# Performance work log

Hardware: AMD Instinct MI355X
Metric: run time of the kernel (lower is better)

## Reference

```python
import jax, jax.numpy as jnp
import numpy as np

EPS = 2e-5
N_ROT = 4  # p4 group: rotations by multiples of 90 degrees (exact via rot90)


def _conv2d(x, w, pad):
    # x: [B, Cin, H, W], w: [Cout, Cin, k, k]
    return jax.lax.conv_general_dilated(
        x, w, window_strides=(1, 1), padding=[(pad, pad), (pad, pad)],
        dimension_numbers=('NCHW', 'OIHW', 'NCHW'))


def _conv_rng(x, w):
    # Lifting (Rn -> G) conv. x: [B, I, H, W], w: [O, I, k, k] -> [B, O, 4, H', W']
    O, I, k, _ = w.shape
    wr = jnp.stack([jnp.rot90(w, r, axes=(-2, -1)) for r in range(N_ROT)])  # [4,O,I,k,k]
    y = _conv2d(x, wr.reshape(N_ROT * O, I, k, k), 0)  # [B, 4*O, H', W']
    B, _, H2, W2 = y.shape
    return y.reshape(B, N_ROT, O, H2, W2).transpose(0, 2, 1, 3, 4)


def _conv_gg(x, w, pad=0):
    # Group (G -> G) conv. x: [B, I, 4, H, W], w: [O, I, 4, k, k] -> [B, O, 4, H', W']
    O, I, _, k, _ = w.shape
    ws = []
    for r in range(N_ROT):
        wr = jnp.rot90(w, r, axes=(-2, -1))      # spatial rotation of the kernel
        wr = jnp.roll(wr, r, axis=2)              # cyclic shift of orientation axis
        ws.append(wr.reshape(O, I * N_ROT, k, k))
    wall = jnp.concatenate(ws, 0)                 # [4*O, I*4, k, k]
    B = x.shape[0]
    y = _conv2d(x.reshape(B, I * N_ROT, x.shape[-2], x.shape[-1]), wall, pad)
    H2, W2 = y.shape[-2:]
    return y.reshape(B, N_ROT, O, H2, W2).transpose(0, 2, 1, 3, 4)


def _att_rng(x, aw):
    # fSpatialAttention on Rn input: channel avg+max pooling -> 7x7 conv -> sigmoid gate.
    # x: [B, C, H, W], aw: [1, 2, 7, 7]
    pooled = jnp.concatenate([x.mean(1, keepdims=True), x.max(1, keepdims=True)], axis=1)
    att = jax.nn.sigmoid(_conv2d(pooled, aw, 3))  # [B,1,H,W], SAME padding
    return x * att


def _att_gg(x, aw):
    # fSpatialAttentionGG on G input: channel avg+max pooling -> equivariant 7x7 GG conv -> sigmoid.
    # x: [B, C, 4, H, W], aw: [1, 2, 4, 7, 7]
    pooled = jnp.concatenate([x.mean(1, keepdims=True), x.max(1, keepdims=True)], axis=1)
    att = jax.nn.sigmoid(_conv_gg(pooled, aw, pad=3))  # [B,1,4,H,W]
    return x * att


def _bn(x, g, b):
    # BatchNorm3d over [B, C, 4, H, W]: per-channel stats over (B, 4, H, W)
    m = x.mean((0, 2, 3, 4), keepdims=True)
    v = x.var((0, 2, 3, 4), keepdims=True)
    return (x - m) * jax.lax.rsqrt(v + EPS) * g.reshape(1, -1, 1, 1, 1) + b.reshape(1, -1, 1, 1, 1)


def _pool(x):
    # max_pooling_Rn: 2x2/2 spatial max pool applied independently per orientation
    return jax.lax.reduce_window(x, -jnp.inf, jax.lax.max,
                                 (1, 1, 1, 2, 2), (1, 1, 1, 2, 2), 'VALID')


def setup_inputs() -> dict:
    key = jax.random.key(0)
    ks = jax.random.split(key, 40)
    B, C = 2048, 10
    d = {'x': jax.random.normal(ks[0], (B, 1, 28, 28), jnp.float32)}
    d['c1_w'] = 0.2 * jax.random.normal(ks[1], (C, 1, 3, 3), jnp.float32)
    d['a1_w'] = 0.1 * jax.random.normal(ks[2], (1, 2, 7, 7), jnp.float32)
    j = 3
    for i in range(2, 7):
        d['c%d_w' % i] = 0.1 * jax.random.normal(ks[j], (C, C, 4, 3, 3), jnp.float32); j += 1
        d['a%d_w' % i] = 0.1 * jax.random.normal(ks[j], (1, 2, 4, 7, 7), jnp.float32); j += 1
    d['c7_w'] = 0.1 * jax.random.normal(ks[j], (10, C, 4, 4, 4), jnp.float32); j += 1
    d['a7_w'] = 0.1 * jax.random.normal(ks[j], (1, 2, 4, 7, 7), jnp.float32); j += 1
    for i in range(1, 7):
        d['bn%d_g' % i] = jnp.ones((C,), jnp.float32)
        d['bn%d_b' % i] = jnp.zeros((C,), jnp.float32)
    return d


def reference(x, c1_w, a1_w, c2_w, a2_w, c3_w, a3_w, c4_w, a4_w, c5_w, a5_w,
              c6_w, a6_w, c7_w, a7_w, bn1_g, bn1_b, bn2_g, bn2_b, bn3_g, bn3_b,
              bn4_g, bn4_b, bn5_g, bn5_b, bn6_g, bn6_b):
    # Dropout is treated as identity (eval mode / deterministic reference).
    out = jax.nn.relu(_bn(_conv_rng(_att_rng(x, a1_w), c1_w), bn1_g, bn1_b))      # [B,10,4,26,26]
    out = jax.nn.relu(_bn(_conv_gg(_att_gg(out, a2_w), c2_w), bn2_g, bn2_b))       # [B,10,4,24,24]
    out = _pool(out)                                                                # [B,10,4,12,12]
    out = jax.nn.relu(_bn(_conv_gg(_att_gg(out, a3_w), c3_w), bn3_g, bn3_b))       # 10x10
    out = jax.nn.relu(_bn(_conv_gg(_att_gg(out, a4_w), c4_w), bn4_g, bn4_b))       # 8x8
    out = jax.nn.relu(_bn(_conv_gg(_att_gg(out, a5_w), c5_w), bn5_g, bn5_b))       # 6x6
    out = jax.nn.relu(_bn(_conv_gg(_att_gg(out, a6_w), c6_w), bn6_g, bn6_b))       # 4x4
    out = _conv_gg(_att_gg(out, a7_w), c7_w)                                        # [B,10,4,1,1]
    out = out.max(axis=2)                                                           # group max-pool over orientations
    return out.reshape(out.shape[0], 10)
```

## Files before the change

kernel.cpp:

```cpp
#include <hip/hip_runtime.h>
#include <hip/hip_bf16.h>
#include <cstddef>

typedef __hip_bfloat16 bf;
typedef __attribute__((ext_vector_type(8))) short short8x;
typedef __attribute__((ext_vector_type(4))) float f32x4;

__device__ __forceinline__ float ldv(const float* p){ return *p; }
__device__ __forceinline__ float ldv(const bf* p){ return __bfloat162float(*p); }
__device__ __forceinline__ void stv(float* p, float v){ *p = v; }
__device__ __forceinline__ void stv(bf* p, float v){ *p = __float2bfloat16(v); }
__device__ __forceinline__ float sigm(float x){ return 1.f/(1.f + __expf(-x)); }
__device__ __forceinline__ short bfbits(float v){
  __hip_bfloat16 h = __float2bfloat16(v);
  return *(short*)&h;
}

__device__ __forceinline__ float ldin(const void* p, long i, int f32){
  return f32 ? ((const float*)p)[i] : __bfloat162float(((const bf*)p)[i]);
}

template<int K>
__device__ __forceinline__ int rot_src(int r, int t){
  int u = t / K, v = t % K;
  int s1 = v*K + (K-1-u);
  int s2 = (K-1-u)*K + (K-1-v);
  int s3 = (K-1-v)*K + u;
  return r==0 ? t : (r==1 ? s1 : (r==2 ? s2 : s3));
}

template<int HW_, int WIN>
__device__ __forceinline__ void conv12x2(const short* __restrict__ xin5, int b0, int b1, int lq,
                                         const short8x (&bm)[9], const short8x (&bt)[3],
                                         const int (&tdh)[3], const int (&tdw)[3],
                                         f32x4& acc0, f32x4& acc1){
  short8x A[9];
  #pragma unroll
  for (int t = 0; t < 9; ++t)
    A[t] = *(const short8x*)&xin5[(lq*HW_ + b0 + (t/3)*WIN + (t%3))*8];
  #pragma unroll
  for (int t = 0; t < 9; ++t)
    acc0 = __builtin_amdgcn_mfma_f32_16x16x32_bf16(A[t], bm[t], acc0, 0, 0, 0);
  #pragma unroll
  for (int tg = 0; tg < 3; ++tg){
    short8x a = *(const short8x*)&xin5[(4*HW_ + b0 + tdh[tg]*WIN + tdw[tg])*8];
    acc0 = __builtin_amdgcn_mfma_f32_16x16x32_bf16(a, bt[tg], acc0, 0, 0, 0);
  }
  #pragma unroll
  for (int t = 0; t < 9; ++t){
    short8x a = *(const short8x*)&xin5[(lq*HW_ + b1 + (t/3)*WIN + (t%3))*8];
    acc1 = __builtin_amdgcn_mfma_f32_16x16x32_bf16(a, bm[t], acc1, 0, 0, 0);
  }
  #pragma unroll
  for (int tg = 0; tg < 3; ++tg){
    short8x a = *(const short8x*)&xin5[(4*HW_ + b1 + tdh[tg]*WIN + tdw[tg])*8];
    acc1 = __builtin_amdgcn_mfma_f32_16x16x32_bf16(a, bt[tg], acc1, 0, 0, 0);
  }
}

__global__ void k_detect(const void* x, int* ctrl){
  int lane = threadIdx.x;
  float mx = 0.f;
  for (int i = lane; i < 2048; i += 64){
    float v = __bfloat162float(((const bf*)x)[i]);
    if (v != v) v = 1e30f;
    mx = fmaxf(mx, fabsf(v));
  }
  #pragma unroll
  for (int off = 32; off > 0; off >>= 1) mx = fmaxf(mx, __shfl_xor(mx, off));
  if (lane == 0) ctrl[0] = (mx > 1e6f) ? 1 : 0;
}

__global__ __launch_bounds__(256) void k_build_bt(const void* c2, const void* c3, const void* c4,
                                                  const int* __restrict__ ctrl, short* __restrict__ btg){
  const void* ws[3] = {c2, c3, c4};
  const void* cw = ws[blockIdx.x];
  short* outp = btg + blockIdx.x * 18432;
  int f32 = ctrl[0];
  for (int i = threadIdx.x; i < 18432; i += 256){
    int t, n, k;
    bool valid;
    if (i < 13824){
      t = i / 1536;
      int rem = i % 1536;
      int kq = rem / 384;
      n = (i >> 3) % 48;
      k = kq*8 + (i & 7);
      valid = (n < 40);
    } else {
      int j2 = i - 13824;
      int tg = j2 / 1536;
      int lq = (j2 % 1536) / 384;
      n = (j2 >> 3) % 48;
      k = 32 + (i & 7);
      t = tg*4 + lq;
      valid = (t < 9) && (n < 40);
    }
    float v = 0.f;
    if (valid){
      int o = n >> 2, r = n & 3, ci = k >> 2, s = k & 3;
      v = ldin(cw, ((o*10 + ci)*4 + ((s - r) & 3))*9 + rot_src<3>(r, t), f32);
    }
    outp[i] = bfbits(v);
  }
}

__global__ __launch_bounds__(256) void k_l1(const void* __restrict__ x,
                                            const void* __restrict__ a1,
                                            const void* __restrict__ c1,
                                            const int* __restrict__ ctrl,
                                            float* __restrict__ xa,
                                            float* __restrict__ ssum, float* __restrict__ ssq){
  __shared__ float xs[784];
  __shared__ float ws[49];
  __shared__ float xg[28*29];
  __shared__ float wr1[360];
  __shared__ float lsum[16], lss[16];
  int b = blockIdx.x, tid = threadIdx.x;
  int f32 = ctrl[0];
  for (int i = tid; i < 784; i += 256) xs[i] = ldin(x, (long)b*784 + i, f32);
  if (tid < 49) ws[tid] = ldin(a1, tid, f32) + ldin(a1, 49 + tid, f32);
  for (int i = tid; i < 360; i += 256){
    int r = i / 90, rem = i % 90, o = rem / 9, t = rem % 9;
    wr1[i] = ldin(c1, o*9 + rot_src<3>(r, t), f32);
  }
  if (tid < 16){ lsum[tid] = 0.f; lss[tid] = 0.f; }
  __syncthreads();
  for (int p = tid; p < 784; p += 256){
    int h = p / 28, w = p % 28;
    float acc = 0.f;
    #pragma unroll
    for (int u = 0; u < 7; ++u){
      int hh = h + u - 3;
      if (hh < 0 || hh >= 28) continue;
      #pragma unroll
      for (int v = 0; v < 7; ++v){
        int ww = w + v - 3;
        if (ww < 0 || ww >= 28) continue;
        acc = fmaf(xs[hh*28 + ww], ws[u*7 + v], acc);
      }
    }
    float g = xs[p] * sigm(acc);
    xg[h*29 + w] = g;
    xa[(size_t)b*784 + p] = g;
  }
  __syncthreads();
  for (int it = tid; it < 1040; it += 256){
    int o = it / 104, rem = it % 104, r = rem / 26, h = rem % 26;
    float wt[9];
    #pragma unroll
    for (int t = 0; t < 9; ++t) wt[t] = wr1[(r*10 + o)*9 + t];
    float acc[26];
    #pragma unroll
    for (int w = 0; w < 26; ++w) acc[w] = 0.f;
    #pragma unroll
    for (int u = 0; u < 3; ++u){
      float rr[28];
      #pragma unroll
      for (int j = 0; j < 28; ++j) rr[j] = xg[(h + u)*29 + j];
      #pragma unroll
      for (int v = 0; v < 3; ++v){
        float wv = wt[u*3 + v];
        #pragma unroll
        for (int w = 0; w < 26; ++w) acc[w] = fmaf(rr[w + v], wv, acc[w]);
      }
    }
    float s1 = 0.f, s2 = 0.f;
    #pragma unroll
    for (int w = 0; w < 26; ++w){ s1 += acc[w]; s2 += acc[w]*acc[w]; }
    atomicAdd(&lsum[o], s1); atomicAdd(&lss[o], s2);
  }
  __syncthreads();
  if (tid < 10){ atomicAdd(&ssum[tid], lsum[tid]); atomicAdd(&ssq[tid], lss[tid]); }
}

__global__ __launch_bounds__(128) void k_att2(const float* __restrict__ xa,
                                              const void* __restrict__ c1,
                                              const float* __restrict__ psum,
                                              const float* __restrict__ psq,
                                              const void* __restrict__ g,
                                              const void* __restrict__ bb,
                                              float invN,
                                              const void* __restrict__ aw,
                                              const int* __restrict__ ctrl,
                                              float* __restrict__ attf){
  __shared__ float xs[28*29];
  __shared__ float wr1[360];
  __shared__ float ps[8*26*33];
  __shared__ float wl[1568];
  __shared__ float scs[10], shs[10];
  int b = blockIdx.x, tid = threadIdx.x;
  int f32 = ctrl[0];
  if (tid < 10){
    float m = psum[tid] * invN;
    float v = fmaxf(psq[tid] * invN - m*m, 0.f);
    float sc = ldin(g, tid, f32) * rsqrtf(v + 2e-5f);
    scs[tid] = sc;
    shs[tid] = ldin(bb, tid, f32) - m * sc;
  }
  for (int i = tid; i < 784; i += 128){
    int row = i / 28, col = i % 28;
    xs[row*29 + col] = xa[(size_t)b*784 + i];
  }
  for (int i = tid; i < 360; i += 128){
    int r = i / 90, rem = i % 90, o = rem / 9, t = rem % 9;
    wr1[i] = ldin(c1, o*9 + rot_src<3>(r, t), f32);
  }
  for (int i = tid; i < 8*26*33; i += 128) ps[i] = 0.f;
  for (int i = tid; i < 1568; i += 128){
    int r = i / 392, rem = i % 392, i2 = rem / 196, s = (rem % 196)/49, t = rem % 49;
    int sp = (s - r) & 3;
    wl[i] = ldin(aw, (i2*4 + sp)*49 + rot_src<7>(r, t), f32);
  }
  __syncthreads();
  if (tid < 104){
    int s = tid / 26, h = tid % 26;
    float msum[26], mmax[26];
    #pragma unroll
    for (int w = 0; w < 26; ++w){ msum[w] = 0.f; mmax[w] = 0.f; }
    for (int o = 0; o < 10; ++o){
      const float* wb = wr1 + (s*10 + o)*9;
      float acc[26];
      #pragma unroll
      for (int w = 0; w < 26; ++w) acc[w] = 0.f;
      #pragma unroll
      for (int u = 0; u < 3; ++u){
        float rr[28];
        #pragma unroll
        for (int j = 0; j < 28; ++j) rr[j] = xs[(h + u)*29 + j];
        #pragma unroll
        for (int v = 0; v < 3; ++v){
          float wv = wb[u*3 + v];
          #pragma unroll
          for (int w = 0; w < 26; ++w) acc[w] = fmaf(rr[w + v], wv, acc[w]);
        }
      }
      float a_sc = scs[o], a_sh = shs[o];
      #pragma unroll
      for (int w = 0; w < 26; ++w){
        float val = fmaxf(fmaf(acc[w], a_sc, a_sh), 0.f);
        msum[w] += val; mmax[w] = fmaxf(mmax[w], val);
      }
    }
    #pragma unroll
    for (int w = 0; w < 26; ++w){
      ps[s*858 + h*33 + 3 + w] = msum[w] * 0.1f;
      ps[(4 + s)*858 + h*33 + 3 + w] = mmax[w];
    }
  }
  __syncthreads();
  if (tid < 104){
    int r = tid / 26, h = tid % 26;
    float acc[26];
    #pragma unroll
    for (int w = 0; w < 26; ++w) acc[w] = 0.f;
    for (int c = 0; c < 8; ++c){
      const float* wb = wl + r*392 + c*49;
      const float* pb = ps + c*858;
      #pragma unroll
      for (int u = 0; u < 7; ++u){
        int row = h + u - 3;
        if (row < 0 || row >= 26) continue;
        float rr[32];
        #pragma unroll
        for (int j = 0; j < 32; ++j) rr[j] = pb[row*33 + j];
        #pragma unroll
        for (int v = 0; v < 7; ++v){
          float wv = wb[u*7 + v];
          #pragma unroll
          for (int w = 0; w < 26; ++w) acc[w] = fmaf(rr[w + v], wv, acc[w]);
        }
      }
    }
    size_t base = ((size_t)b*4 + r)*676 + (size_t)h*26;
    #pragma unroll
    for (int w = 0; w < 26; ++w) attf[base + w] = sigm(acc[w]);
  }
}

__global__ __launch_bounds__(512, 4) void k_conv2m(const float* __restrict__ xa,
                                                const void* __restrict__ c1,
                                                const float* __restrict__ psum,
                                                const float* __restrict__ psq,
                                                const void* __restrict__ g,
                                                const void* __restrict__ bb,
                                                float invN,
                                                const float* __restrict__ attm,
                                                const short* __restrict__ btg,
                                                const int* __restrict__ ctrl,
                                                bf* __restrict__ ap2,
                                                float* __restrict__ ssum, float* __restrict__ ssq){
  __shared__ alignas(16) float xs2[784];
  __shared__ float wr1[360];
  __shared__ alignas(16) float attL[4*676];
  __shared__ alignas(16) short xin5[5*676*8];
  __shared__ float lsum[16], lss[16];
  __shared__ float scs[10], shs[10];
  int tid = threadIdx.x, b = blockIdx.x;
  int f32 = ctrl[0];
  if (tid < 10){
    float m = psum[tid] * invN;
    float v = fmaxf(psq[tid] * invN - m*m, 0.f);
    float sc = ldin(g, tid, f32) * rsqrtf(v + 2e-5f);
    scs[tid] = sc;
    shs[tid] = ldin(bb, tid, f32) - m * sc;
  }
  for (int i = tid; i < 784; i += 512) xs2[i] = xa[(size_t)b*784 + i];
  for (int i = tid; i < 360; i += 512){
    int r = i / 90, rem = i % 90, o = rem / 9, t = rem % 9;
    wr1[i] = ldin(c1, o*9 + rot_src<3>(r, t), f32);
  }
  for (int i = tid; i < 2704; i += 512) attL[i] = attm[(size_t)b*2704 + i];
  if (tid < 16){ lsum[tid] = 0.f; lss[tid] = 0.f; }
  __syncthreads();
  for (int it = tid; it < 1040; it += 512){
    int row = it / 40, ch = it % 40;
    int ci = ch >> 2, s = ch & 3;
    float wt[9];
    {
      const float* wb = wr1 + (s*10 + ci)*9;
      #pragma unroll
      for (int t = 0; t < 9; ++t) wt[t] = wb[t];
    }
    float sc = scs[ci], sh = shs[ci];
    float acc[26];
    #pragma unroll
    for (int w = 0; w < 26; ++w) acc[w] = 0.f;
    #pragma unroll
    for (int u = 0; u < 3; ++u){
      float rr[28];
      const float4* rp = (const float4*)(xs2 + (row + u)*28);
      #pragma unroll
      for (int j = 0; j < 7; ++j){ float4 q = rp[j]; rr[4*j]=q.x; rr[4*j+1]=q.y; rr[4*j+2]=q.z; rr[4*j+3]=q.w; }
      #pragma unroll
      for (int v = 0; v < 3; ++v){
        float wv = wt[u*3 + v];
        #pragma unroll
        for (int w = 0; w < 26; ++w) acc[w] = fmaf(rr[w + v], wv, acc[w]);
      }
    }
    const float* ap = attL + s*676 + row*26;
    int gbase = (ch >> 3)*676 + row*26;
    int c7 = ch & 7;
    #pragma unroll
    for (int w = 0; w < 26; ++w){
      float v = fmaxf(fmaf(acc[w], sc, sh), 0.f) * ap[w];
      xin5[(gbase + w)*8 + c7] = bfbits(v);
    }
  }
  __syncthreads();

  int wv = tid >> 6, lane = tid & 63, lm = lane & 15, lq = lane >> 4;
  short8x bmain[9], btail[3];
  int tdh[3], tdw[3];
  #pragma unroll
  for (int tg = 0; tg < 3; ++tg){
    int tap = tg*4 + lq; if (tap > 8) tap = 8;
    tdh[tg] = tap / 3; tdw[tg] = tap % 3;
  }
  int curNt = -1, n = 0, o = 0;
  for (int u = wv; u < 54; u += 8){
    int nt = u / 18, mp = u % 18;
    if (nt != curNt){
      curNt = nt; n = nt*16 + lm; o = n >> 2;
      #pragma unroll
      for (int t = 0; t < 9; ++t)
        bmain[t] = *(const short8x*)(btg + (((t*4 + lq)*48 + n) << 3));
      #pragma unroll
      for (int tg = 0; tg < 3; ++tg)
        btail[tg] = *(const short8x*)(btg + 13824 + (((tg*4 + lq)*48 + n) << 3));
    }
    int mt0 = mp*2, mt1 = mp*2 + 1;
    int mA0 = mt0*16 + lm, mA1 = mt1*16 + lm;
    int qi0 = mA0 >> 2, sub0 = mA0 & 3;
    int h00 = 2*(qi0/12) + (sub0 >> 1), w00 = 2*(qi0%12) + (sub0 & 1);
    int qi1 = mA1 >> 2, sub1 = mA1 & 3;
    int h01 = 2*(qi1/12) + (sub1 >> 1), w01 = 2*(qi1%12) + (sub1 & 1);
    f32x4 acc0 = {0.f,0.f,0.f,0.f}, acc1 = {0.f,0.f,0.f,0.f};
    conv12x2<676,26>(xin5, h00*26 + w00, h01*26 + w01, lq, bmain, btail, tdh, tdw, acc0, acc1);
    if (n < 40){
      float s1 = acc0[0]+acc0[1]+acc0[2]+acc0[3] + acc1[0]+acc1[1]+acc1[2]+acc1[3];
      float s2 = acc0[0]*acc0[0]+acc0[1]*acc0[1]+acc0[2]*acc0[2]+acc0[3]*acc0[3]
               + acc1[0]*acc1[0]+acc1[1]*acc1[1]+acc1[2]*acc1[2]+acc1[3]*acc1[3];
      atomicAdd(&lsum[o], s1); atomicAdd(&lss[o], s2);
      float mx0 = fmaxf(fmaxf(acc0[0], acc0[1]), fmaxf(acc0[2], acc0[3]));
      float mx1 = fmaxf(fmaxf(acc1[0], acc1[1]), fmaxf(acc1[2], acc1[3]));
      size_t pbase = ((size_t)b*40 + n)*144;
      stv(ap2 + pbase + mt0*4 + lq, mx0);
      stv(ap2 + pbase + mt1*4 + lq, mx1);
    }
  }
  __syncthreads();
  if (tid < 10){ atomicAdd(&ssum[tid], lsum[tid]); atomicAdd(&ssq[tid], lss[tid]); }
}

template<int HIN, int NT, typename TI>
__global__ __launch_bounds__(NT) void k_conv_ggm(const TI* __restrict__ act,
                                                 const float* __restrict__ psum,
                                                 const float* __restrict__ psq,
                                                 const void* __restrict__ g,
                                                 const void* __restrict__ bb,
                                                 float invN,
                                                 const float* __restrict__ attm,
                                                 const short* __restrict__ btg,
                                                 const int* __restrict__ ctrl,
                                                 float* __restrict__ out,
                                                 float* __restrict__ ssum, float* __restrict__ ssq){
  constexpr int WIN = HIN, HOUT = HIN - 2, WOUT = WIN - 2;
  constexpr int M = HOUT*WOUT, HW = HIN*WIN;
  constexpr int MT = (M + 15)/16, MU = (MT + 1)/2, UNITS = MU*3;
  constexpr int NWV = NT/64;
  __shared__ alignas(16) short xin5[5*HW*8];
  __shared__ float lsum[16], lss[16];
  __shared__ float scs[10], shs[10];
  int tid = threadIdx.x, b = blockIdx.x;
  int f32 = ctrl[0];
  if (tid < 10){
    float m = psum[tid]*invN;
    float v = fmaxf(psq[tid]*invN - m*m, 0.f);
    float sc = ldin(g, tid, f32)*rsqrtf(v + 2e-5f);
    scs[tid] = sc; shs[tid] = ldin(bb, tid, f32) - m*sc;
  }
  if (tid < 16){ lsum[tid] = 0.f; lss[tid] = 0.f; }
  __syncthreads();
  for (int i = tid; i < HW*40; i += NT){
    int sp = i / 40, ch = i % 40;
    int ci = ch >> 2, s = ch & 3;
    float a = ldv(act + ((size_t)b*40 + ch)*HW + sp);
    a = fmaxf(fmaf(a, scs[ci], shs[ci]), 0.f);
    float v = a * attm[((size_t)b*4 + s)*HW + sp];
    xin5[((ch >> 3)*HW + sp)*8 + (ch & 7)] = bfbits(v);
  }
  __syncthreads();
  int wv = tid >> 6, lane = tid & 63, lm = lane & 15, lq = lane >> 4;
  short8x bmain[9], btail[3];
  int tdh[3], tdw[3];
  #pragma unroll
  for (int tg = 0; tg < 3; ++tg){
    int tap = tg*4 + lq; if (tap > 8) tap = 8;
    tdh[tg] = tap / 3; tdw[tg] = tap % 3;
  }
  int curNt = -1, n = 0, o = 0;
  for (int u = wv; u < UNITS; u += NWV){
    int nt = u / MU, mu = u % MU;
    if (nt != curNt){
      curNt = nt; n = nt*16 + lm; o = n >> 2;
      #pragma unroll
      for (int t = 0; t < 9; ++t)
        bmain[t] = *(const short8x*)(btg + (((t*4 + lq)*48 + n) << 3));
      #pragma unroll
      for (int tg = 0; tg < 3; ++tg)
        btail[tg] = *(const short8x*)(btg + 13824 + (((tg*4 + lq)*48 + n) << 3));
    }
    int mt0 = mu*2, mt1 = mu*2 + 1;
    int mA0 = mt0*16 + lm; if (mA0 > M-1) mA0 = M-1;
    int mA1 = mt1*16 + lm; if (mA1 > M-1) mA1 = M-1;
    int base0 = (mA0 / WOUT)*WIN + (mA0 % WOUT);
    int base1 = (mA1 / WOUT)*WIN + (mA1 % WOUT);
    f32x4 acc0 = {0.f,0.f,0.f,0.f}, acc1 = {0.f,0.f,0.f,0.f};
    conv12x2<HW,WIN>(xin5, base0, base1, lq, bmain, btail, tdh, tdw, acc0, acc1);
    if (n < 40){
      float s1 = 0.f, s2 = 0.f;
      size_t obase = ((size_t)b*40 + n)*M;
      #pragma unroll
      for (int reg = 0; reg < 4; ++reg){
        int m0 = mt0*16 + lq*4 + reg;
        if (m0 < M){ float v = acc0[reg]; s1 += v; s2 += v*v; out[obase + m0] = v; }
        int m1 = mt1*16 + lq*4 + reg;
        if (m1 < M){ float v = acc1[reg]; s1 += v; s2 += v*v; out[obase + m1] = v; }
      }
      atomicAdd(&lsum[o], s1); atomicAdd(&lss[o], s2);
    }
  }
  __syncthreads();
  if (tid < 10){ atomicAdd(&ssum[tid], lsum[tid]); atomicAdd(&ssq[tid], lss[tid]); }
}

template<int H, int W, int NT, typename TA>
__global__ __launch_bounds__(NT) void k_att_gg(const TA* __restrict__ act,
                                               const float* __restrict__ psum,
                                               const float* __restrict__ psq,
                                               const void* __restrict__ g,
                                               const void* __restrict__ bb,
                                               float invN,
                                               const void* __restrict__ aw,
                                               const int* __restrict__ ctrl,
                                               float* __restrict__ att){
  constexpr int WG = (W + 6) | 1;
  constexpr int HW = H*W;
  __shared__ float ps[8*H*WG];
  __shared__ float wl[1568];
  __shared__ float scs[10], shs[10];
  int b = blockIdx.x, tid = threadIdx.x;
  int f32 = ctrl[0];
  if (tid < 10){
    float m = psum[tid]*invN;
    float v = fmaxf(psq[tid]*invN - m*m, 0.f);
    float sc = ldin(g, tid, f32)*rsqrtf(v + 2e-5f);
    scs[tid] = sc; shs[tid] = ldin(bb, tid, f32) - m*sc;
  }
  for (int i = tid; i < 1568; i += NT){
    int r = i / 392, rem = i % 392, i2 = rem / 196, s = (rem % 196)/49, t = rem % 49;
    int sp = (s - r) & 3;
    wl[i] = ldin(aw, (i2*4 + sp)*49 + rot_src<7>(r, t), f32);
  }
  __syncthreads();
  for (int i = tid; i < 4*H*WG; i += NT){
    int s = i / (H*WG), rem = i % (H*WG), row = rem / WG, col = rem % WG;
    int cc = col - 3;
    float mn = 0.f, mx = 0.f;
    if (cc >= 0 && cc < W){
      float sum = 0.f; mx = 0.f;
      const TA* ap = act + (size_t)b*40*HW + (size_t)s*HW + row*W + cc;
      #pragma unroll
      for (int c = 0; c < 10; ++c){
        float v = fmaxf(fmaf(ldv(ap + (size_t)c*4*HW), scs[c], shs[c]), 0.f);
        sum += v; mx = fmaxf(mx, v);
      }
      mn = sum * 0.1f;
    }
    ps[s*H*WG + row*WG + col] = mn;
    ps[(4 + s)*H*WG + row*WG + col] = mx;
  }
  __syncthreads();
  for (int it = tid; it < 4*H; it += NT){
    int r = it / H, h = it % H;
    float acc[W];
    #pragma unroll
    for (int w = 0; w < W; ++w) acc[w] = 0.f;
    for (int c = 0; c < 8; ++c){
      const float* wb = wl + r*392 + c*49;
      const float* pb = ps + c*H*WG;
      #pragma unroll
      for (int u = 0; u < 7; ++u){
        int row = h + u - 3;
        if (row < 0 || row >= H) continue;
        float rr[W + 6];
        #pragma unroll
        for (int j = 0; j < W + 6; ++j) rr[j] = pb[row*WG + j];
        #pragma unroll
        for (int v = 0; v < 7; ++v){
          float wv = wb[u*7 + v];
          #pragma unroll
          for (int w = 0; w < W; ++w) acc[w] = fmaf(rr[w + v], wv, acc[w]);
        }
      }
    }
    size_t base = ((size_t)b*4 + r)*HW + (size_t)h*W;
    #pragma unroll
    for (int w = 0; w < W; ++w) att[base + w] = sigm(acc[w]);
  }
}

template<int HIN, int K, int SR, int NT, bool STATS, bool FINAL, typename TI>
__global__ __launch_bounds__(NT) void k_conv_gg(const TI* __restrict__ act,
                                                const float* __restrict__ psum,
                                                const float* __restrict__ psq,
                                                const void* __restrict__ g,
                                                const void* __restrict__ bb,
                                                float invN,
                                                const float* __restrict__ attm,
                                                const void* __restrict__ cw,
                                                const int* __restrict__ ctrl,
                                                void* __restrict__ out,
                                                float* __restrict__ ssum, float* __restrict__ ssq){
  constexpr int WIN  = HIN;
  constexpr int HOUT = HIN - K + 1;
  constexpr int WOUT = WIN - K + 1;
  constexpr int NS   = HOUT / SR;
  constexpr int WP   = WIN | 1;
  constexpr int NW   = 10*10*4*K*K;
  constexpr int HW   = HIN*WIN;
  __shared__ float xin[40*HIN*WP];
  __shared__ float wl[NW];
  __shared__ float lsum[16], lss[16];
  __shared__ float scs[10], shs[10];
  __shared__ float red[48];
  int tid = threadIdx.x;
  int b = blockIdx.x;
  int f32 = ctrl[0];
  if (tid < 10){
    float m = psum[tid]*invN;
    float v = fmaxf(psq[tid]*invN - m*m, 0.f);
    float sc = ldin(g, tid, f32)*rsqrtf(v + 2e-5f);
    scs[tid] = sc; shs[tid] = ldin(bb, tid, f32) - m*sc;
  }
  if (STATS && tid < 16){ lsum[tid] = 0.f; lss[tid] = 0.f; }
  for (int i = tid; i < NW; i += NT) wl[i] = ldin(cw, i, f32);
  __syncthreads();
  for (int i = tid; i < 40*HIN*WP; i += NT){
    int c = i / (HIN*WP), rem = i % (HIN*WP), rr = rem / WP, col = rem % WP;
    float v = 0.f;
    if (col < WIN){
      int ch = c >> 2, s = c & 3;
      float a = ldv(act + ((size_t)b*40 + c)*HW + (size_t)rr*WIN + col);
      a = fmaxf(fmaf(a, scs[ch], shs[ch]), 0.f);
      v = a * attm[((size_t)b*4 + s)*HW + (size_t)rr*WIN + col];
    }
    xin[i] = v;
  }
  __syncthreads();
  for (int it = tid; it < 40*NS; it += NT){
    int o = it / (4*NS), rem = it % (4*NS), r = rem / NS, hs = rem % NS;
    int h0 = hs * SR;
    int perm[K*K];
    #pragma unroll
    for (int t = 0; t < K*K; ++t) perm[t] = rot_src<K>(r, t);
    float acc[SR][WOUT];
    #pragma unroll
    for (int a = 0; a < SR; ++a)
      #pragma unroll
      for (int w = 0; w < WOUT; ++w) acc[a][w] = 0.f;
    for (int ci = 0; ci < 10; ++ci){
      #pragma unroll
      for (int s = 0; s < 4; ++s){
        int sp = (s - r) & 3;
        const float* wb = wl + (size_t)((o*10 + ci)*4 + sp)*K*K;
        float wt[K*K];
        #pragma unroll
        for (int t = 0; t < K*K; ++t) wt[t] = wb[perm[t]];
        const float* ib = xin + (ci*4 + s)*HIN*WP;
        #pragma unroll
        for (int ri = 0; ri < SR + K - 1; ++ri){
          float rr3[WP];
          #pragma unroll
          for (int j = 0; j < WP; ++j) rr3[j] = ib[(h0 + ri)*WP + j];
          #pragma unroll
          for (int u = 0; u < K; ++u){
            int orr = ri - u;
            if (orr < 0 || orr >= SR) continue;
            #pragma unroll
            for (int v = 0; v < K; ++v){
              float wv = wt[u*K + v];
              #pragma unroll
              for (int w = 0; w < WOUT; ++w) acc[orr][w] = fmaf(rr3[w + v], wv, acc[orr][w]);
            }
          }
        }
      }
    }
    if constexpr (STATS){
      float s1 = 0.f, s2 = 0.f;
      #pragma unroll
      for (int a = 0; a < SR; ++a)
        #pragma unroll
        for (int w = 0; w < WOUT; ++w){ s1 += acc[a][w]; s2 += acc[a][w]*acc[a][w]; }
      atomicAdd(&lsum[o], s1); atomicAdd(&lss[o], s2);
    }
    if constexpr (FINAL){
      red[o*4 + r] = acc[0][0];
    } else {
      #pragma unroll
      for (int a = 0; a < SR; ++a){
        size_t base = ((size_t)b*40 + o*4 + r)*HOUT*WOUT + (size_t)(h0 + a)*WOUT;
        #pragma unroll
        for (int w = 0; w < WOUT; ++w) ((float*)out)[base + w] = acc[a][w];
      }
    }
  }
  if constexpr (STATS){
    __syncthreads();
    if (tid < 10){ atomicAdd(&ssum[tid], lsum[tid]); atomicAdd(&ssq[tid], lss[tid]); }
  }
  if constexpr (FINAL){
    __syncthreads();
    if (tid < 10){
      float m4 = fmaxf(fmaxf(red[tid*4], red[tid*4+1]), fmaxf(red[tid*4+2], red[tid*4+3]));
      if (f32) ((float*)out)[(size_t)b*10 + tid] = m4;
      else stv((bf*)out + (size_t)b*10 + tid, m4);
    }
  }
}

extern "C" void kernel_launch(void* const* d_in, const int* in_sizes, int n_in,
                              void* d_out, int out_size, void* d_ws, size_t ws_size,
                              hipStream_t stream){
  (void)in_sizes; (void)n_in; (void)out_size; (void)ws_size;
  const void* x  = d_in[0];
  const void* c1 = d_in[1];
  const void* a1 = d_in[2];
  const void* c2 = d_in[3];
  const void* a2 = d_in[4];
  const void* c3 = d_in[5];
  const void* a3 = d_in[6];
  const void* c4 = d_in[7];
  const void* a4 = d_in[8];
  const void* c5 = d_in[9];
  const void* a5 = d_in[10];
  const void* c6 = d_in[11];
  const void* a6 = d_in[12];
  const void* c7 = d_in[13];
  const void* a7 = d_in[14];
  const void* bng[6] = {d_in[15],d_in[17],d_in[19],d_in[21],d_in[23],d_in[25]};
  const void* bnb[6] = {d_in[16],d_in[18],d_in[20],d_in[22],d_in[24],d_in[26]};

  size_t off = 0;
  char* wsb = (char*)d_ws;
  auto alloc = [&](size_t bytes)->void*{ void* p = wsb + off; off += (bytes + 255) & ~(size_t)255; return p; };
  int*   ctrl   = (int*)alloc(256);
  float* stats  = (float*)alloc(192*sizeof(float));
  float* scales = (float*)alloc(192*sizeof(float));
  (void)scales;
  short* btfr   = (short*)alloc(3*18432*2);
  char*  region1 = (char*)alloc(28573696);
  bf*    ap2 = (bf*)alloc((size_t)2048*40*144*2);
  float* yD  = (float*)alloc((size_t)2048*40*100*4);
  float* xa    = (float*)region1;
  float* attf2 = (float*)(region1 + 6422528);
  float* yE    = (float*)region1;
  float* attf3 = (float*)(region1 + 20971520);

  hipMemsetAsync(ctrl, 0, 1024, stream);
  k_detect<<<1, 64, 0, stream>>>(x, ctrl);
  k_build_bt<<<3, 256, 0, stream>>>(c2, c3, c4, ctrl, btfr);

  k_l1<<<2048, 256, 0, stream>>>(x, a1, c1, ctrl, xa, stats + 0, stats + 16);

  k_att2<<<2048, 128, 0, stream>>>(xa, c1, stats + 0, stats + 16, bng[0], bnb[0],
                                   1.f/5537792.f, a2, ctrl, attf2);
  k_conv2m<<<2048, 512, 0, stream>>>(xa, c1, stats + 0, stats + 16, bng[0], bnb[0],
                                     1.f/5537792.f, attf2, btfr, ctrl, ap2, stats + 32, stats + 48);

  k_att_gg<12,12,64,bf><<<2048, 64, 0, stream>>>(ap2, stats + 32, stats + 48, bng[1], bnb[1],
                                                 1.f/4718592.f, a3, ctrl, attf3);
  k_conv_ggm<12,256,bf><<<2048, 256, 0, stream>>>(ap2, stats + 32, stats + 48, bng[1], bnb[1],
                                                  1.f/4718592.f, attf3, btfr + 18432, ctrl,
                                                  yD, stats + 64, stats + 80);

  k_att_gg<10,10,64,float><<<2048, 64, 0, stream>>>(yD, stats + 64, stats + 80, bng[2], bnb[2],
                                                    1.f/819200.f, a4, ctrl, attf3);
  k_conv_ggm<10,128,float><<<2048, 128, 0, stream>>>(yD, stats + 64, stats + 80, bng[2], bnb[2],
                                                     1.f/819200.f, attf3, btfr + 36864, ctrl,
                                                     yE, stats + 96, stats + 112);

  k_att_gg<8,8,64,float><<<2048, 64, 0, stream>>>(yE, stats + 96, stats + 112, bng[3], bnb[3],
                                                  1.f/524288.f, a5, ctrl, attf3);
  k_conv_gg<8,3,2,192,true,false,float><<<2048, 192, 0, stream>>>(yE, stats + 96, stats + 112,
                                                  bng[3], bnb[3], 1.f/524288.f, attf3, c5, ctrl,
                                                  yD, stats + 128, stats + 144);

  k_att_gg<6,6,64,float><<<2048, 64, 0, stream>>>(yD, stats + 128, stats + 144, bng[4], bnb[4],
                                                  1.f/294912.f, a6, ctrl, attf3);
  k_conv_gg<6,3,2,128,true,false,float><<<2048, 128, 0, stream>>>(yD, stats + 128, stats + 144,
                                                  bng[4], bnb[4], 1.f/294912.f, attf3, c6, ctrl,
                                                  yE, stats + 160, stats + 176);

  k_att_gg<4,4,64,float><<<2048, 64, 0, stream>>>(yE, stats + 160, stats + 176, bng[5], bnb[5],
                                                  1.f/131072.f, a7, ctrl, attf3);
  k_conv_gg<4,4,1,64,false,true,float><<<2048, 64, 0, stream>>>(yE, stats + 160, stats + 176,
                                                  bng[5], bnb[5], 1.f/131072.f, attf3, c7, ctrl,
                                                  d_out, (float*)nullptr, (float*)nullptr);
}
```

Before: 966.9 us.

## Swizzle LDS activation layout for MFMA loads and split k_att2 rows across threads

Applies an XOR swizzle to the 16-byte activation slots in shared memory used by the MFMA conv kernels, on both the store and the load side, to reduce LDS bank conflicts. The shared buffers are padded up to a multiple of 8 slots so swizzled indices stay in bounds. Separately, k_att2 now runs 256 threads with each row split into two halves of 13 columns, doubling active threads and cutting per-thread register arrays. Risks include swizzle inconsistency between the writers and readers, and extra index arithmetic on every load.

```diff
diff --git a/kernel.cpp b/kernel.cpp
--- a/kernel.cpp
+++ b/kernel.cpp
@@ -20,6 +20,8 @@
   return f32 ? ((const float*)p)[i] : __bfloat162float(((const bf*)p)[i]);
 }
 
+__device__ __forceinline__ int swz(int u){ return u ^ ((u >> 3) & 7); }
+
 template<int K>
 __device__ __forceinline__ int rot_src(int r, int t){
   int u = t / K, v = t % K;
@@ -37,23 +39,23 @@
   short8x A[9];
   #pragma unroll
   for (int t = 0; t < 9; ++t)
-    A[t] = *(const short8x*)&xin5[(lq*HW_ + b0 + (t/3)*WIN + (t%3))*8];
+    A[t] = *(const short8x*)&xin5[swz(lq*HW_ + b0 + (t/3)*WIN + (t%3))*8];
   #pragma unroll
   for (int t = 0; t < 9; ++t)
     acc0 = __builtin_amdgcn_mfma_f32_16x16x32_bf16(A[t], bm[t], acc0, 0, 0, 0);
   #pragma unroll
   for (int tg = 0; tg < 3; ++tg){
-    short8x a = *(const short8x*)&xin5[(4*HW_ + b0 + tdh[tg]*WIN + tdw[tg])*8];
+    short8x a = *(const short8x*)&xin5[swz(4*HW_ + b0 + tdh[tg]*WIN + tdw[tg])*8];
     acc0 = __builtin_amdgcn_mfma_f32_16x16x32_bf16(a, bt[tg], acc0, 0, 0, 0);
   }
   #pragma unroll
   for (int t = 0; t < 9; ++t){
-    short8x a = *(const short8x*)&xin5[(lq*HW_ + b1 + (t/3)*WIN + (t%3))*8];
+    short8x a = *(const short8x*)&xin5[swz(lq*HW_ + b1 + (t/3)*WIN + (t%3))*8];
     acc1 = __builtin_amdgcn_mfma_f32_16x16x32_bf16(a, bm[t], acc1, 0, 0, 0);
   }
   #pragma unroll
   for (int tg = 0; tg < 3; ++tg){
-    short8x a = *(const short8x*)&xin5[(4*HW_ + b1 + tdh[tg]*WIN + tdw[tg])*8];
+    short8x a = *(const short8x*)&xin5[swz(4*HW_ + b1 + tdh[tg]*WIN + tdw[tg])*8];
     acc1 = __builtin_amdgcn_mfma_f32_16x16x32_bf16(a, bt[tg], acc1, 0, 0, 0);
   }
 }
@@ -174,7 +176,7 @@
   if (tid < 10){ atomicAdd(&ssum[tid], lsum[tid]); atomicAdd(&ssq[tid], lss[tid]); }
 }
 
-__global__ __launch_bounds__(128) void k_att2(const float* __restrict__ xa,
+__global__ __launch_bounds__(256) void k_att2(const float* __restrict__ xa,
                                               const void* __restrict__ c1,
                                               const float* __restrict__ psum,
                                               const float* __restrict__ psq,
@@ -198,62 +200,66 @@
     scs[tid] = sc;
     shs[tid] = ldin(bb, tid, f32) - m * sc;
   }
-  for (int i = tid; i < 784; i += 128){
+  for (int i = tid; i < 784; i += 256){
     int row = i / 28, col = i % 28;
     xs[row*29 + col] = xa[(size_t)b*784 + i];
   }
-  for (int i = tid; i < 360; i += 128){
+  for (int i = tid; i < 360; i += 256){
     int r = i / 90, rem = i % 90, o = rem / 9, t = rem % 9;
     wr1[i] = ldin(c1, o*9 + rot_src<3>(r, t), f32);
   }
-  for (int i = tid; i < 8*26*33; i += 128) ps[i] = 0.f;
-  for (int i = tid; i < 1568; i += 128){
+  for (int i = tid; i < 8*26*33; i += 256) ps[i] = 0.f;
+  for (int i = tid; i < 1568; i += 256){
     int r = i / 392, rem = i % 392, i2 = rem / 196, s = (rem % 196)/49, t = rem % 49;
     int sp = (s - r) & 3;
     wl[i] = ldin(aw, (i2*4 + sp)*49 + rot_src<7>(r, t), f32);
   }
   __syncthreads();
-  if (tid < 104){
-    int s = tid / 26, h = tid % 26;
-    float msum[26], mmax[26];
-    #pragma unroll
-    for (int w = 0; w < 26; ++w){ msum[w] = 0.f; mmax[w] = 0.f; }
+  if (tid < 208){
+    int pair = tid >> 1, half = tid & 1;
+    int s = pair / 26, h = pair % 26;
+    int w0 = half*13;
+    float msum[13], mmax[13];
+    #pragma unroll
+    for (int w = 0; w < 13; ++w){ msum[w] = 0.f; mmax[w] = 0.f; }
     for (int o = 0; o < 10; ++o){
       const float* wb = wr1 + (s*10 + o)*9;
-      float acc[26];
-      #pragma unroll
-      for (int w = 0; w < 26; ++w) acc[w] = 0.f;
+      float acc[13];
+      #pragma unroll
+      for (int w = 0; w < 13; ++w) acc[w] = 0.f;
       #pragma unroll
       for (int u = 0; u < 3; ++u){
-        float rr[28];
-        #pragma unroll
-        for (int j = 0; j < 28; ++j) rr[j] = xs[(h + u)*29 + j];
+        float rr[15];
+        #pragma unroll
+        for (int j = 0; j < 15; ++j) rr[j] = xs[(h + u)*29 + w0 + j];
         #pragma unroll
         for (int v = 0; v < 3; ++v){
           float wv = wb[u*3 + v];
           #pragma unroll
-          for (int w = 0; w < 26; ++w) acc[w] = fmaf(rr[w + v], wv, acc[w]);
+          for (int w = 0; w < 13; ++w) acc[w] = fmaf(rr[w + v], wv, acc[w]);
         }
       }
       float a_sc = scs[o], a_sh = shs[o];
       #pragma unroll
-      for (int w = 0; w < 26; ++w){
+      for (int w = 0; w < 13; ++w){
         float val = fmaxf(fmaf(acc[w], a_sc, a_sh), 0.f);
         msum[w] += val; mmax[w] = fmaxf(mmax[w], val);
       }
     }
     #pragma unroll
-    for (int w = 0; w < 26; ++w){
-      ps[s*858 + h*33 + 3 + w] = msum[w] * 0.1f;
-      ps[(4 + s)*858 + h*33 + 3 + w] = mmax[w];
-    }
-  }
-  __syncthreads();
-  if (tid < 104){
-    int r = tid / 26, h = tid % 26;
-    float acc[26];
-    #pragma unroll
-    for (int w = 0; w < 26; ++w) acc[w] = 0.f;
+    for (int w = 0; w < 13; ++w){
+      ps[s*858 + h*33 + 3 + w0 + w] = msum[w] * 0.1f;
+      ps[(4 + s)*858 + h*33 + 3 + w0 + w] = mmax[w];
+    }
+  }
+  __syncthreads();
+  if (tid < 208){
+    int pair = tid >> 1, half = tid & 1;
+    int r = pair / 26, h = pair % 26;
+    int w0 = half*13;
+    float acc[13];
+    #pragma unroll
+    for (int w = 0; w < 13; ++w) acc[w] = 0.f;
     for (int c = 0; c < 8; ++c){
       const float* wb = wl + r*392 + c*49;
       const float* pb = ps + c*858;
@@ -261,20 +267,20 @@
       for (int u = 0; u < 7; ++u){
         int row = h + u - 3;
         if (row < 0 || row >= 26) continue;
-        float rr[32];
-        #pragma unroll
-        for (int j = 0; j < 32; ++j) rr[j] = pb[row*33 + j];
+        float rr[19];
+        #pragma unroll
+        for (int j = 0; j < 19; ++j) rr[j] = pb[row*33 + w0 + j];
         #pragma unroll
         for (int v = 0; v < 7; ++v){
           float wv = wb[u*7 + v];
           #pragma unroll
-          for (int w = 0; w < 26; ++w) acc[w] = fmaf(rr[w + v], wv, acc[w]);
+          for (int w = 0; w < 13; ++w) acc[w] = fmaf(rr[w + v], wv, acc[w]);
         }
       }
     }
-    size_t base = ((size_t)b*4 + r)*676 + (size_t)h*26;
-    #pragma unroll
-    for (int w = 0; w < 26; ++w) attf[base + w] = sigm(acc[w]);
+    size_t base = ((size_t)b*4 + r)*676 + (size_t)h*26 + w0;
+    #pragma unroll
+    for (int w = 0; w < 13; ++w) attf[base + w] = sigm(acc[w]);
   }
 }
 
@@ -293,7 +299,7 @@
   __shared__ alignas(16) float xs2[784];
   __shared__ float wr1[360];
   __shared__ alignas(16) float attL[4*676];
-  __shared__ alignas(16) short xin5[5*676*8];
+  __shared__ alignas(16) short xin5[3384*8];
   __shared__ float lsum[16], lss[16];
   __shared__ float scs[10], shs[10];
   int tid = threadIdx.x, b = blockIdx.x;
@@ -345,7 +351,7 @@
     #pragma unroll
     for (int w = 0; w < 26; ++w){
       float v = fmaxf(fmaf(acc[w], sc, sh), 0.f) * ap[w];
-      xin5[(gbase + w)*8 + c7] = bfbits(v);
+      xin5[swz(gbase + w)*8 + c7] = bfbits(v);
     }
   }
   __syncthreads();
@@ -410,7 +416,8 @@
   constexpr int M = HOUT*WOUT, HW = HIN*WIN;
   constexpr int MT = (M + 15)/16, MU = (MT + 1)/2, UNITS = MU*3;
   constexpr int NWV = NT/64;
-  __shared__ alignas(16) short xin5[5*HW*8];
+  constexpr int UP = ((5*HW + 7)/8)*8;
+  __shared__ alignas(16) short xin5[UP*8];
   __shared__ float lsum[16], lss[16];
   __shared__ float scs[10], shs[10];
   int tid = threadIdx.x, b = blockIdx.x;
@@ -429,7 +436,7 @@
     float a = ldv(act + ((size_t)b*40 + ch)*HW + sp);
     a = fmaxf(fmaf(a, scs[ci], shs[ci]), 0.f);
     float v = a * attm[((size_t)b*4 + s)*HW + sp];
-    xin5[((ch >> 3)*HW + sp)*8 + (ch & 7)] = bfbits(v);
+    xin5[swz((ch >> 3)*HW + sp)*8 + (ch & 7)] = bfbits(v);
   }
   __syncthreads();
   int wv = tid >> 6, lane = tid & 63, lm = lane & 15, lq = lane >> 4;
@@ -716,7 +723,7 @@
 
   k_l1<<<2048, 256, 0, stream>>>(x, a1, c1, ctrl, xa, stats + 0, stats + 16);
 
-  k_att2<<<2048, 128, 0, stream>>>(xa, c1, stats + 0, stats + 16, bng[0], bnb[0],
+  k_att2<<<2048, 256, 0, stream>>>(xa, c1, stats + 0, stats + 16, bng[0], bnb[0],
                                    1.f/5537792.f, a2, ctrl, attf2);
   k_conv2m<<<2048, 512, 0, stream>>>(xa, c1, stats + 0, stats + 16, bng[0], bnb[0],
                                      1.f/5537792.f, attf2, btfr, ctrl, ap2, stats + 32, stats + 48);
```

Result: faster. 928.8 us (-3.9%).
